# Kernel optimization log

Measured on AMD Instinct MI355X. Metric: run time of the kernel, lower is better.

## Reference

```python
import jax, jax.numpy as jnp
import numpy as np

NUM_HEADS = 8
HEAD_DIM = 64
WIN = (8, 8, 8)  # (wT, wH, wW)


def setup_inputs() -> dict:
    key = jax.random.key(0)
    k1, k2, k3 = jax.random.split(key, 3)
    B, T, H, W, C = 2, 16, 32, 32, 512
    d_inner = NUM_HEADS * HEAD_DIM  # 512
    x = jax.random.normal(k1, (B, T * H * W, C), dtype=jnp.float32)
    # torch Linear weights stored transposed as [in, out] for y = x @ w
    w_qkv = jax.random.normal(k2, (C, 3 * d_inner), dtype=jnp.float32) * (C ** -0.5)
    w_proj = jax.random.normal(k3, (d_inner, C), dtype=jnp.float32) * (d_inner ** -0.5)
    b_proj = jnp.zeros((C,), dtype=jnp.float32)
    return {"x": x, "w_qkv": w_qkv, "w_proj": w_proj, "b_proj": b_proj,
            "T": T, "H": H, "W": W}


def reference(x, w_qkv, w_proj, b_proj, T, H, W):
    B, N, C = x.shape
    wT, wH, wW = WIN
    scale = HEAD_DIM ** -0.5
    # module re-derives T if N mismatches T*H*W
    if N != T * H * W:
        T = N // (H * W)
    xv = x.reshape(B, T, H, W, C)
    pt, ph, pw = (-T) % wT, (-H) % wH, (-W) % wW
    if pt or ph or pw:
        xv = jnp.pad(xv, ((0, 0), (0, pt), (0, ph), (0, pw), (0, 0)))
    Tp, Hp, Wp = T + pt, H + ph, W + pw
    nT, nH, nW = Tp // wT, Hp // wH, Wp // wW
    L = wT * wH * wW  # tokens per window
    # window partition: [B*nT*nH*nW, L, C]
    xw = xv.reshape(B, nT, wT, nH, wH, nW, wW, C)
    xw = xw.transpose(0, 1, 3, 5, 2, 4, 6, 7).reshape(-1, L, C)
    # qkv projection (no bias)
    qkv = xw @ w_qkv  # [nw, L, 3*nh*hd]
    q, k, v = jnp.split(qkv, 3, axis=-1)

    def heads(t):
        return t.reshape(t.shape[0], L, NUM_HEADS, HEAD_DIM).transpose(0, 2, 1, 3)

    q, k, v = heads(q), heads(k), heads(v)  # [nw, h, L, d]
    attn = jax.nn.softmax(jnp.einsum('nhid,nhjd->nhij', q, k) * scale, axis=-1)
    o = jnp.einsum('nhij,nhjd->nhid', attn, v)
    o = o.transpose(0, 2, 1, 3).reshape(-1, L, NUM_HEADS * HEAD_DIM)
    o = o @ w_proj + b_proj  # output projection
    # window un-partition
    o = o.reshape(B, nT, nH, nW, wT, wH, wW, C)
    o = o.transpose(0, 1, 4, 2, 5, 3, 6, 7).reshape(B, Tp, Hp, Wp, C)
    return o[:, :T, :H, :W].reshape(B, N, C)
```

## Files before the change

### kernel.cpp

```cpp
#include <hip/hip_runtime.h>
#include <hip/hip_bf16.h>

typedef __hip_bfloat16 bf16;
typedef __attribute__((ext_vector_type(8))) short bf16x8;
typedef __attribute__((ext_vector_type(4))) float f32x4;

#define MROWS 32768
#define CDIM 512
#define SEL_STRIDE (512*512*64)

__device__ __forceinline__ int win_to_src_row(int m) {
  int win = m >> 9, l = m & 511;
  int b = win >> 5, rr = win & 31;
  int nt = rr >> 4, nh = (rr >> 2) & 3, nw = rr & 3;
  int wt = l >> 6, wh = (l >> 3) & 7, ww = l & 7;
  int tt = nt * 8 + wt, hh = nh * 8 + wh, wp = nw * 8 + ww;
  return (b << 14) + (tt << 10) + (hh << 5) + wp;
}

__device__ __forceinline__ unsigned short bf16bits(bf16 h) {
  return __builtin_bit_cast(unsigned short, h);
}

__device__ __forceinline__ int xcd_chunk(int bx, int n) {
  return (bx & 7) * (n >> 3) + (bx >> 3);
}

__global__ __launch_bounds__(256) void transpose_cvt_kernel(
    const float* __restrict__ src, bf16* __restrict__ dst, int R, int C) {
  __shared__ float tile[32][33];
  int bc = blockIdx.x * 32, br = blockIdx.y * 32;
  int tx = threadIdx.x, ty = threadIdx.y;
#pragma unroll
  for (int i = 0; i < 32; i += 8)
    tile[ty + i][tx] = src[(size_t)(br + ty + i) * C + bc + tx];
  __syncthreads();
#pragma unroll
  for (int i = 0; i < 32; i += 8)
    dst[(size_t)(bc + ty + i) * R + br + tx] = __float2bfloat16(tile[tx][ty + i]);
}

__global__ __launch_bounds__(256) void perm_x_kernel(const float* __restrict__ x,
                                                     bf16* __restrict__ xw) {
  const int total = MROWS * (CDIM / 4);
  for (int i = blockIdx.x * 256 + threadIdx.x; i < total; i += 2048 * 256) {
    int m = i >> 7, c4 = (i & 127) * 4;
    int src = win_to_src_row(m);
    float4 v = *(const float4*)(x + (size_t)src * CDIM + c4);
    ushort4 o;
    o.x = bf16bits(__float2bfloat16(v.x));
    o.y = bf16bits(__float2bfloat16(v.y));
    o.z = bf16bits(__float2bfloat16(v.z));
    o.w = bf16bits(__float2bfloat16(v.w));
    *(ushort4*)(xw + (size_t)m * CDIM + c4) = o;
  }
}

#define BM 128
#define BN 128
#define BK 64

__device__ __forceinline__ void gload16(const bf16* g, bf16* l) {
  __builtin_amdgcn_global_load_lds(
      (const __attribute__((address_space(1))) unsigned int*)g,
      (__attribute__((address_space(3))) unsigned int*)l, 16, 0, 0);
}

template <int MODE>
__global__ __launch_bounds__(256) void gemm_bt_kernel(
    const bf16* __restrict__ A, const bf16* __restrict__ Bt, int Ntiles,
    bf16* __restrict__ qkv_out, float* __restrict__ out,
    const float* __restrict__ bias) {
  __shared__ __align__(16) bf16 Asl[BM * BK];
  __shared__ __align__(16) bf16 Bsl[BN * BK];
  const int K = 512;
  int l2 = xcd_chunk(blockIdx.x, gridDim.x);
  int bn = (l2 >> 3) % Ntiles;
  int bm = (l2 & 7) + (l2 / (8 * Ntiles)) * 8;
  int t = threadIdx.x, lane = t & 63, w = t >> 6;
  int wr = w >> 1, wc = w & 1;
  int l15 = lane & 15, lh = lane >> 4;
  f32x4 acc[4][4] = {};

  for (int kt = 0; kt < K; kt += BK) {
    __syncthreads();
#pragma unroll
    for (int i = 0; i < 4; ++i) {
      int f = i * 256 + t;
      int row = f >> 3, cb = f & 7;
      gload16(A + (size_t)(bm * BM + row) * K + kt + cb * 8,
              &Asl[(i * 256 + w * 64) * 8]);
    }
#pragma unroll
    for (int i = 0; i < 4; ++i) {
      int f = i * 256 + t;
      int row = f >> 3, cb = f & 7;
      gload16(Bt + (size_t)(bn * BN + row) * K + kt + cb * 8,
              &Bsl[(i * 256 + w * 64) * 8]);
    }
    __syncthreads();
#pragma unroll
    for (int kk = 0; kk < 2; ++kk) {
      bf16x8 af[4], bfr[4];
#pragma unroll
      for (int mi = 0; mi < 4; ++mi)
        af[mi] = *(const bf16x8*)&Asl[(wr * 64 + mi * 16 + l15) * BK + kk * 32 + lh * 8];
#pragma unroll
      for (int nj = 0; nj < 4; ++nj)
        bfr[nj] = *(const bf16x8*)&Bsl[(wc * 64 + nj * 16 + l15) * BK + kk * 32 + lh * 8];
#pragma unroll
      for (int mi = 0; mi < 4; ++mi)
#pragma unroll
        for (int nj = 0; nj < 4; ++nj)
          acc[mi][nj] = __builtin_amdgcn_mfma_f32_16x16x32_bf16(
              af[mi], bfr[nj], acc[mi][nj], 0, 0, 0);
    }
  }

  if (MODE == 0) {
#pragma unroll
    for (int mi = 0; mi < 4; ++mi) {
      int row = bm * BM + wr * 64 + mi * 16 + lh * 4;
      int win = row >> 9, tok = row & 511;
#pragma unroll
      for (int nj = 0; nj < 4; ++nj) {
        int col = bn * BN + wc * 64 + nj * 16 + l15;
        int sel = col >> 9, cc = col & 511;
        int head = cc >> 6, d = cc & 63;
        if (sel == 2) {
          ushort4 pk;
          pk.x = bf16bits(__float2bfloat16(acc[mi][nj][0]));
          pk.y = bf16bits(__float2bfloat16(acc[mi][nj][1]));
          pk.z = bf16bits(__float2bfloat16(acc[mi][nj][2]));
          pk.w = bf16bits(__float2bfloat16(acc[mi][nj][3]));
          *(ushort4*)(qkv_out + 2 * (size_t)SEL_STRIDE +
                      (((size_t)(win * 8 + head)) * 64 + d) * 512 + tok) = pk;
        } else {
          size_t base = (size_t)sel * SEL_STRIDE +
                        (((size_t)(win * 8 + head)) * 512 + tok) * 64 + d;
#pragma unroll
          for (int r = 0; r < 4; ++r)
            qkv_out[base + (size_t)r * 64] = __float2bfloat16(acc[mi][nj][r]);
        }
      }
    }
  } else {
#pragma unroll
    for (int mi = 0; mi < 4; ++mi) {
      int row = bm * BM + wr * 64 + mi * 16 + lh * 4;
#pragma unroll
      for (int r = 0; r < 4; ++r) {
        int srow = win_to_src_row(row + r);
        float* op = out + (size_t)srow * CDIM;
#pragma unroll
        for (int nj = 0; nj < 4; ++nj) {
          int col = bn * BN + wc * 64 + nj * 16 + l15;
          op[col] = acc[mi][nj][r] + bias[col];
        }
      }
    }
  }
}

__global__ __launch_bounds__(256, 2) void attn_kernel(const bf16* __restrict__ qkv_ws,
                                                      bf16* __restrict__ o_ws) {
  __shared__ __align__(16) bf16 Pl[4][4][16 * 64];
  int l2 = xcd_chunk(blockIdx.x, 1024);
  int wh = l2 >> 1, qc = l2 & 1;
  int win = wh >> 3, head = wh & 7;
  int t = threadIdx.x, lane = t & 63, w = t >> 6;
  int l15 = lane & 15, lh = lane >> 4;
  const bf16* qb = qkv_ws + (size_t)wh * (512 * 64);
  const bf16* kb = qb + SEL_STRIDE;
  const bf16* vtb = qkv_ws + 2 * (size_t)SEL_STRIDE + (size_t)wh * (64 * 512);

  const float c_scale = 0.18033688011112042f;
  int q0 = qc * 256 + w * 64;
  bf16x8 qf[4][2];
#pragma unroll
  for (int qi = 0; qi < 4; ++qi)
#pragma unroll
    for (int kk = 0; kk < 2; ++kk)
      qf[qi][kk] = *(const bf16x8*)(qb + (size_t)(q0 + qi * 16 + l15) * 64 + kk * 32 + lh * 8);

  f32x4 acco[4][4] = {};
  float lsum[4][4] = {};
  for (int kt = 0; kt < 8; ++kt) {
    bf16x8 kf[4][2], vf[4][2];
#pragma unroll
    for (int kj = 0; kj < 4; ++kj) {
      int tok = kt * 64 + kj * 16 + l15;
#pragma unroll
      for (int kk = 0; kk < 2; ++kk)
        kf[kj][kk] = *(const bf16x8*)(kb + (size_t)tok * 64 + kk * 32 + lh * 8);
    }
#pragma unroll
    for (int nj = 0; nj < 4; ++nj) {
      int d = nj * 16 + l15;
#pragma unroll
      for (int kk = 0; kk < 2; ++kk)
        vf[nj][kk] = *(const bf16x8*)(vtb + (size_t)d * 512 + kt * 64 + kk * 32 + lh * 8);
    }
#pragma unroll
    for (int qi = 0; qi < 4; ++qi) {
      f32x4 s[4] = {};
#pragma unroll
      for (int kj = 0; kj < 4; ++kj)
#pragma unroll
        for (int kk = 0; kk < 2; ++kk)
          s[kj] = __builtin_amdgcn_mfma_f32_16x16x32_bf16(qf[qi][kk], kf[kj][kk], s[kj], 0, 0, 0);
#pragma unroll
      for (int kj = 0; kj < 4; ++kj)
#pragma unroll
        for (int r = 0; r < 4; ++r) {
          float p = __builtin_exp2f(s[kj][r] * c_scale);
          s[kj][r] = p;
          lsum[qi][r] += p;
        }
#pragma unroll
      for (int kj = 0; kj < 4; ++kj)
#pragma unroll
        for (int r = 0; r < 4; ++r) {
          int prow = lh * 4 + r, pcol = kj * 16 + l15;
          *(bf16*)((char*)&Pl[w][qi][0] + prow * 128 + ((pcol * 2) ^ ((prow & 7) << 4))) =
              __float2bfloat16(s[kj][r]);
        }
      bf16x8 pa[2];
#pragma unroll
      for (int kk = 0; kk < 2; ++kk)
        pa[kk] = *(const bf16x8*)((const char*)&Pl[w][qi][0] + l15 * 128 +
                                  ((kk * 64 + lh * 16) ^ ((l15 & 7) << 4)));
#pragma unroll
      for (int nj = 0; nj < 4; ++nj)
#pragma unroll
        for (int kk = 0; kk < 2; ++kk)
          acco[qi][nj] = __builtin_amdgcn_mfma_f32_16x16x32_bf16(pa[kk], vf[nj][kk],
                                                                 acco[qi][nj], 0, 0, 0);
    }
  }
#pragma unroll
  for (int qi = 0; qi < 4; ++qi) {
    float inv[4];
#pragma unroll
    for (int r = 0; r < 4; ++r) {
      float v = lsum[qi][r];
      v += __shfl_xor(v, 1);
      v += __shfl_xor(v, 2);
      v += __shfl_xor(v, 4);
      v += __shfl_xor(v, 8);
      inv[r] = __frcp_rn(v);
    }
#pragma unroll
    for (int nj = 0; nj < 4; ++nj)
#pragma unroll
      for (int r = 0; r < 4; ++r) {
        int row = q0 + qi * 16 + lh * 4 + r;
        int d = nj * 16 + l15;
        o_ws[((size_t)win * 512 + row) * 512 + head * 64 + d] =
            __float2bfloat16(acco[qi][nj][r] * inv[r]);
      }
  }
}

extern "C" void kernel_launch(void* const* d_in, const int* in_sizes, int n_in,
                              void* d_out, int out_size, void* d_ws, size_t ws_size,
                              hipStream_t stream) {
  const float* x = (const float*)d_in[0];
  const float* w_qkv = (const float*)d_in[1];
  const float* w_proj = (const float*)d_in[2];
  const float* b_proj = (const float*)d_in[3];
  float* out = (float*)d_out;

  const size_t OFF_QKV = 33554432;
  const size_t OFF_WQ = OFF_QKV + 100663296;
  const size_t OFF_WP = OFF_WQ + 1572864;
  const size_t NEED = OFF_WP + 524288;
  if (ws_size < NEED) return;

  char* ws = (char*)d_ws;
  bf16* xw = (bf16*)ws;
  bf16* qkv = (bf16*)(ws + OFF_QKV);
  bf16* wqkvT = (bf16*)(ws + OFF_WQ);
  bf16* wprojT = (bf16*)(ws + OFF_WP);
  bf16* o_ws = xw;

  transpose_cvt_kernel<<<dim3(1536 / 32, 512 / 32), dim3(32, 8), 0, stream>>>(w_qkv, wqkvT, 512, 1536);
  transpose_cvt_kernel<<<dim3(512 / 32, 512 / 32), dim3(32, 8), 0, stream>>>(w_proj, wprojT, 512, 512);
  perm_x_kernel<<<2048, 256, 0, stream>>>(x, xw);
  gemm_bt_kernel<0><<<256 * 12, 256, 0, stream>>>(xw, wqkvT, 12, qkv, nullptr, nullptr);
  attn_kernel<<<1024, 256, 0, stream>>>(qkv, o_ws);
  gemm_bt_kernel<1><<<256 * 4, 256, 0, stream>>>(o_ws, wprojT, 4, nullptr, out, b_proj);
}
```

Baseline: 233.3 us.

## Fuse QKV projection into attention kernel, keeping Q/K/V in LDS

Replaces the separate QKV GEMM plus attention kernels with one kernel per (window, head) that computes Q, K and V from the permuted input straight into shared memory, then runs the attention. This removes the round trip of a large bf16 QKV intermediate through global memory and one launch. In exchange each block re-reads the whole window's input twice, there are only 512 blocks of 512 threads using 160KB of LDS, and there is no cross-head reuse of the input tiles.

```diff
diff --git a/kernel.cpp b/kernel.cpp
--- a/kernel.cpp
+++ b/kernel.cpp
@@ -7,7 +7,6 @@
 
 #define MROWS 32768
 #define CDIM 512
-#define SEL_STRIDE (512*512*64)
 
 __device__ __forceinline__ int win_to_src_row(int m) {
   int win = m >> 9, l = m & 511;
@@ -20,6 +19,15 @@
 
 __device__ __forceinline__ unsigned short bf16bits(bf16 h) {
   return __builtin_bit_cast(unsigned short, h);
+}
+
+__device__ __forceinline__ ushort4 pack4(f32x4 a) {
+  ushort4 o;
+  o.x = bf16bits(__float2bfloat16(a[0]));
+  o.y = bf16bits(__float2bfloat16(a[1]));
+  o.z = bf16bits(__float2bfloat16(a[2]));
+  o.w = bf16bits(__float2bfloat16(a[3]));
+  return o;
 }
 
 __device__ __forceinline__ int xcd_chunk(int bx, int n) {
@@ -56,21 +64,203 @@
   }
 }
 
+__device__ __forceinline__ void gload16(const bf16* g, const bf16* l) {
+  __builtin_amdgcn_global_load_lds(
+      (const __attribute__((address_space(1))) unsigned int*)g,
+      (__attribute__((address_space(3))) unsigned int*)l, 16, 0, 0);
+}
+
+__global__ __launch_bounds__(512, 2) void fused_qkv_attn_kernel(
+    const bf16* __restrict__ xw, const bf16* __restrict__ wqkvT,
+    bf16* __restrict__ o_ws) {
+  __shared__ __align__(16) char smem[163840];
+  bf16* Xl = (bf16*)smem;
+  char* Kl = smem + 32768;
+  char* Vl = smem + 98304;
+  char* Ql = Vl;
+
+  int wh = xcd_chunk(blockIdx.x, 512);
+  int win = wh >> 3, head = wh & 7;
+  int t = threadIdx.x, lane = t & 63, w = t >> 6;
+  int l15 = lane & 15, lh = lane >> 4;
+  const bf16* xb = xw + (size_t)win * (512 * 512);
+
+  f32x4 aqk[8][4] = {};
+  for (int kt = 0; kt < 16; ++kt) {
+    bf16x8 aW[8];
+#pragma unroll
+    for (int mi = 0; mi < 8; ++mi) {
+      int wrow = (mi < 4 ? head * 64 + mi * 16 : 512 + head * 64 + (mi - 4) * 16) + l15;
+      aW[mi] = *(const bf16x8*)(wqkvT + (size_t)wrow * 512 + kt * 32 + lh * 8);
+    }
+    __syncthreads();
+#pragma unroll
+    for (int i = 0; i < 4; ++i) {
+      int f = i * 512 + t;
+      int row = f >> 2, cb = f & 3;
+      gload16(xb + (size_t)row * 512 + kt * 32 + (cb ^ (row & 3)) * 8,
+              (const bf16*)((char*)Xl + (i * 512 + w * 64) * 16));
+    }
+    __syncthreads();
+    bf16x8 bX[4];
+#pragma unroll
+    for (int ti = 0; ti < 4; ++ti) {
+      int row = w * 64 + ti * 16 + l15;
+      bX[ti] = *(const bf16x8*)((const char*)Xl + row * 64 + ((lh * 16) ^ ((row & 3) << 4)));
+    }
+#pragma unroll
+    for (int mi = 0; mi < 8; ++mi)
+#pragma unroll
+      for (int ti = 0; ti < 4; ++ti)
+        aqk[mi][ti] = __builtin_amdgcn_mfma_f32_16x16x32_bf16(aW[mi], bX[ti], aqk[mi][ti], 0, 0, 0);
+  }
+#pragma unroll
+  for (int mi = 0; mi < 8; ++mi)
+#pragma unroll
+    for (int ti = 0; ti < 4; ++ti) {
+      int tok = w * 64 + ti * 16 + l15;
+      int d0 = (mi & 3) * 16 + lh * 4;
+      char* base = (mi < 4) ? Ql : Kl;
+      *(ushort4*)(base + tok * 128 + ((d0 * 2) ^ ((tok & 7) << 4))) = pack4(aqk[mi][ti]);
+    }
+  __syncthreads();
+  bf16x8 qf[4][2];
+#pragma unroll
+  for (int qi = 0; qi < 4; ++qi) {
+    int tok = w * 64 + qi * 16 + l15;
+#pragma unroll
+    for (int kk = 0; kk < 2; ++kk)
+      qf[qi][kk] = *(const bf16x8*)(Ql + tok * 128 + ((kk * 64 + lh * 16) ^ ((tok & 7) << 4)));
+  }
+  __syncthreads();
+
+  f32x4 av[4][4] = {};
+  for (int kt = 0; kt < 16; ++kt) {
+    bf16x8 bW[4];
+#pragma unroll
+    for (int nj = 0; nj < 4; ++nj) {
+      int wrow = 1024 + head * 64 + nj * 16 + l15;
+      bW[nj] = *(const bf16x8*)(wqkvT + (size_t)wrow * 512 + kt * 32 + lh * 8);
+    }
+    __syncthreads();
+#pragma unroll
+    for (int i = 0; i < 4; ++i) {
+      int f = i * 512 + t;
+      int row = f >> 2, cb = f & 3;
+      gload16(xb + (size_t)row * 512 + kt * 32 + (cb ^ (row & 3)) * 8,
+              (const bf16*)((char*)Xl + (i * 512 + w * 64) * 16));
+    }
+    __syncthreads();
+    bf16x8 aX[4];
+#pragma unroll
+    for (int ti = 0; ti < 4; ++ti) {
+      int row = w * 64 + ti * 16 + l15;
+      aX[ti] = *(const bf16x8*)((const char*)Xl + row * 64 + ((lh * 16) ^ ((row & 3) << 4)));
+    }
+#pragma unroll
+    for (int ti = 0; ti < 4; ++ti)
+#pragma unroll
+      for (int nj = 0; nj < 4; ++nj)
+        av[ti][nj] = __builtin_amdgcn_mfma_f32_16x16x32_bf16(aX[ti], bW[nj], av[ti][nj], 0, 0, 0);
+  }
+#pragma unroll
+  for (int ti = 0; ti < 4; ++ti)
+#pragma unroll
+    for (int nj = 0; nj < 4; ++nj) {
+      int d = nj * 16 + l15;
+      int tok0 = w * 64 + ti * 16 + lh * 4;
+      *(ushort4*)(Vl + d * 1024 + ((tok0 * 2) ^ ((d & 7) << 4))) = pack4(av[ti][nj]);
+    }
+  __syncthreads();
+
+  const float c_scale = 0.18033688011112042f;
+  int q0 = w * 64;
+  f32x4 acco[4][4] = {};
+  float lsum[4][4] = {};
+  for (int kt = 0; kt < 8; ++kt) {
+    bf16x8 kf[4][2], vf[4][2];
+#pragma unroll
+    for (int kj = 0; kj < 4; ++kj) {
+      int tok = kt * 64 + kj * 16 + l15;
+#pragma unroll
+      for (int kk = 0; kk < 2; ++kk)
+        kf[kj][kk] = *(const bf16x8*)(Kl + tok * 128 + ((kk * 64 + lh * 16) ^ ((tok & 7) << 4)));
+    }
+#pragma unroll
+    for (int nj = 0; nj < 4; ++nj) {
+      int d = nj * 16 + l15;
+#pragma unroll
+      for (int kk = 0; kk < 2; ++kk)
+        vf[nj][kk] = *(const bf16x8*)(Vl + d * 1024 + ((kt * 128 + kk * 64 + lh * 16) ^ ((d & 7) << 4)));
+    }
+#pragma unroll
+    for (int qi = 0; qi < 4; ++qi) {
+      f32x4 s[4] = {};
+#pragma unroll
+      for (int kj = 0; kj < 4; ++kj)
+#pragma unroll
+        for (int kk = 0; kk < 2; ++kk)
+          s[kj] = __builtin_amdgcn_mfma_f32_16x16x32_bf16(qf[qi][kk], kf[kj][kk], s[kj], 0, 0, 0);
+#pragma unroll
+      for (int kj = 0; kj < 4; ++kj)
+#pragma unroll
+        for (int r = 0; r < 4; ++r) {
+          float p = __builtin_exp2f(s[kj][r] * c_scale);
+          s[kj][r] = p;
+          lsum[qi][r] += p;
+        }
+      char* myP = smem + w * 4096 + (qi & 1) * 2048;
+#pragma unroll
+      for (int kj = 0; kj < 4; ++kj)
+#pragma unroll
+        for (int r = 0; r < 4; ++r) {
+          int prow = lh * 4 + r, pcol = kj * 16 + l15;
+          *(bf16*)(myP + prow * 128 + ((pcol * 2) ^ ((prow & 7) << 4))) =
+              __float2bfloat16(s[kj][r]);
+        }
+      bf16x8 pa[2];
+#pragma unroll
+      for (int kk = 0; kk < 2; ++kk)
+        pa[kk] = *(const bf16x8*)(myP + l15 * 128 + ((kk * 64 + lh * 16) ^ ((l15 & 7) << 4)));
+#pragma unroll
+      for (int nj = 0; nj < 4; ++nj)
+#pragma unroll
+        for (int kk = 0; kk < 2; ++kk)
+          acco[qi][nj] = __builtin_amdgcn_mfma_f32_16x16x32_bf16(pa[kk], vf[nj][kk],
+                                                                 acco[qi][nj], 0, 0, 0);
+    }
+  }
+#pragma unroll
+  for (int qi = 0; qi < 4; ++qi) {
+    float inv[4];
+#pragma unroll
+    for (int r = 0; r < 4; ++r) {
+      float v = lsum[qi][r];
+      v += __shfl_xor(v, 1);
+      v += __shfl_xor(v, 2);
+      v += __shfl_xor(v, 4);
+      v += __shfl_xor(v, 8);
+      inv[r] = __frcp_rn(v);
+    }
+#pragma unroll
+    for (int nj = 0; nj < 4; ++nj)
+#pragma unroll
+      for (int r = 0; r < 4; ++r) {
+        int row = q0 + qi * 16 + lh * 4 + r;
+        int d = nj * 16 + l15;
+        o_ws[((size_t)win * 512 + row) * 512 + head * 64 + d] =
+            __float2bfloat16(acco[qi][nj][r] * inv[r]);
+      }
+  }
+}
+
 #define BM 128
 #define BN 128
 #define BK 64
 
-__device__ __forceinline__ void gload16(const bf16* g, bf16* l) {
-  __builtin_amdgcn_global_load_lds(
-      (const __attribute__((address_space(1))) unsigned int*)g,
-      (__attribute__((address_space(3))) unsigned int*)l, 16, 0, 0);
-}
-
-template <int MODE>
-__global__ __launch_bounds__(256) void gemm_bt_kernel(
+__global__ __launch_bounds__(256) void proj_gemm_kernel(
     const bf16* __restrict__ A, const bf16* __restrict__ Bt, int Ntiles,
-    bf16* __restrict__ qkv_out, float* __restrict__ out,
-    const float* __restrict__ bias) {
+    float* __restrict__ out, const float* __restrict__ bias) {
   __shared__ __align__(16) bf16 Asl[BM * BK];
   __shared__ __align__(16) bf16 Bsl[BN * BK];
   const int K = 512;
@@ -88,15 +278,13 @@
     for (int i = 0; i < 4; ++i) {
       int f = i * 256 + t;
       int row = f >> 3, cb = f & 7;
-      gload16(A + (size_t)(bm * BM + row) * K + kt + cb * 8,
-              &Asl[(i * 256 + w * 64) * 8]);
+      gload16(A + (size_t)(bm * BM + row) * K + kt + cb * 8, &Asl[(i * 256 + w * 64) * 8]);
     }
 #pragma unroll
     for (int i = 0; i < 4; ++i) {
       int f = i * 256 + t;
       int row = f >> 3, cb = f & 7;
-      gload16(Bt + (size_t)(bn * BN + row) * K + kt + cb * 8,
-              &Bsl[(i * 256 + w * 64) * 8]);
+      gload16(Bt + (size_t)(bn * BN + row) * K + kt + cb * 8, &Bsl[(i * 256 + w * 64) * 8]);
     }
     __syncthreads();
 #pragma unroll
@@ -112,153 +300,22 @@
       for (int mi = 0; mi < 4; ++mi)
 #pragma unroll
         for (int nj = 0; nj < 4; ++nj)
-          acc[mi][nj] = __builtin_amdgcn_mfma_f32_16x16x32_bf16(
-              af[mi], bfr[nj], acc[mi][nj], 0, 0, 0);
-    }
-  }
-
-  if (MODE == 0) {
-#pragma unroll
-    for (int mi = 0; mi < 4; ++mi) {
-      int row = bm * BM + wr * 64 + mi * 16 + lh * 4;
-      int win = row >> 9, tok = row & 511;
+          acc[mi][nj] = __builtin_amdgcn_mfma_f32_16x16x32_bf16(af[mi], bfr[nj], acc[mi][nj], 0, 0, 0);
+    }
+  }
+#pragma unroll
+  for (int mi = 0; mi < 4; ++mi) {
+    int row = bm * BM + wr * 64 + mi * 16 + lh * 4;
+#pragma unroll
+    for (int r = 0; r < 4; ++r) {
+      int srow = win_to_src_row(row + r);
+      float* op = out + (size_t)srow * CDIM;
 #pragma unroll
       for (int nj = 0; nj < 4; ++nj) {
         int col = bn * BN + wc * 64 + nj * 16 + l15;
-        int sel = col >> 9, cc = col & 511;
-        int head = cc >> 6, d = cc & 63;
-        if (sel == 2) {
-          ushort4 pk;
-          pk.x = bf16bits(__float2bfloat16(acc[mi][nj][0]));
-          pk.y = bf16bits(__float2bfloat16(acc[mi][nj][1]));
-          pk.z = bf16bits(__float2bfloat16(acc[mi][nj][2]));
-          pk.w = bf16bits(__float2bfloat16(acc[mi][nj][3]));
-          *(ushort4*)(qkv_out + 2 * (size_t)SEL_STRIDE +
-                      (((size_t)(win * 8 + head)) * 64 + d) * 512 + tok) = pk;
-        } else {
-          size_t base = (size_t)sel * SEL_STRIDE +
-                        (((size_t)(win * 8 + head)) * 512 + tok) * 64 + d;
-#pragma unroll
-          for (int r = 0; r < 4; ++r)
-            qkv_out[base + (size_t)r * 64] = __float2bfloat16(acc[mi][nj][r]);
-        }
+        op[col] = acc[mi][nj][r] + bias[col];
       }
     }
-  } else {
-#pragma unroll
-    for (int mi = 0; mi < 4; ++mi) {
-      int row = bm * BM + wr * 64 + mi * 16 + lh * 4;
-#pragma unroll
-      for (int r = 0; r < 4; ++r) {
-        int srow = win_to_src_row(row + r);
-        float* op = out + (size_t)srow * CDIM;
-#pragma unroll
-        for (int nj = 0; nj < 4; ++nj) {
-          int col = bn * BN + wc * 64 + nj * 16 + l15;
-          op[col] = acc[mi][nj][r] + bias[col];
-        }
-      }
-    }
-  }
-}
-
-__global__ __launch_bounds__(256, 2) void attn_kernel(const bf16* __restrict__ qkv_ws,
-                                                      bf16* __restrict__ o_ws) {
-  __shared__ __align__(16) bf16 Pl[4][4][16 * 64];
-  int l2 = xcd_chunk(blockIdx.x, 1024);
-  int wh = l2 >> 1, qc = l2 & 1;
-  int win = wh >> 3, head = wh & 7;
-  int t = threadIdx.x, lane = t & 63, w = t >> 6;
-  int l15 = lane & 15, lh = lane >> 4;
-  const bf16* qb = qkv_ws + (size_t)wh * (512 * 64);
-  const bf16* kb = qb + SEL_STRIDE;
-  const bf16* vtb = qkv_ws + 2 * (size_t)SEL_STRIDE + (size_t)wh * (64 * 512);
-
-  const float c_scale = 0.18033688011112042f;
-  int q0 = qc * 256 + w * 64;
-  bf16x8 qf[4][2];
-#pragma unroll
-  for (int qi = 0; qi < 4; ++qi)
-#pragma unroll
-    for (int kk = 0; kk < 2; ++kk)
-      qf[qi][kk] = *(const bf16x8*)(qb + (size_t)(q0 + qi * 16 + l15) * 64 + kk * 32 + lh * 8);
-
-  f32x4 acco[4][4] = {};
-  float lsum[4][4] = {};
-  for (int kt = 0; kt < 8; ++kt) {
-    bf16x8 kf[4][2], vf[4][2];
-#pragma unroll
-    for (int kj = 0; kj < 4; ++kj) {
-      int tok = kt * 64 + kj * 16 + l15;
-#pragma unroll
-      for (int kk = 0; kk < 2; ++kk)
-        kf[kj][kk] = *(const bf16x8*)(kb + (size_t)tok * 64 + kk * 32 + lh * 8);
-    }
-#pragma unroll
-    for (int nj = 0; nj < 4; ++nj) {
-      int d = nj * 16 + l15;
-#pragma unroll
-      for (int kk = 0; kk < 2; ++kk)
-        vf[nj][kk] = *(const bf16x8*)(vtb + (size_t)d * 512 + kt * 64 + kk * 32 + lh * 8);
-    }
-#pragma unroll
-    for (int qi = 0; qi < 4; ++qi) {
-      f32x4 s[4] = {};
-#pragma unroll
-      for (int kj = 0; kj < 4; ++kj)
-#pragma unroll
-        for (int kk = 0; kk < 2; ++kk)
-          s[kj] = __builtin_amdgcn_mfma_f32_16x16x32_bf16(qf[qi][kk], kf[kj][kk], s[kj], 0, 0, 0);
-#pragma unroll
-      for (int kj = 0; kj < 4; ++kj)
-#pragma unroll
-        for (int r = 0; r < 4; ++r) {
-          float p = __builtin_exp2f(s[kj][r] * c_scale);
-          s[kj][r] = p;
-          lsum[qi][r] += p;
-        }
-#pragma unroll
-      for (int kj = 0; kj < 4; ++kj)
-#pragma unroll
-        for (int r = 0; r < 4; ++r) {
-          int prow = lh * 4 + r, pcol = kj * 16 + l15;
-          *(bf16*)((char*)&Pl[w][qi][0] + prow * 128 + ((pcol * 2) ^ ((prow & 7) << 4))) =
-              __float2bfloat16(s[kj][r]);
-        }
-      bf16x8 pa[2];
-#pragma unroll
-      for (int kk = 0; kk < 2; ++kk)
-        pa[kk] = *(const bf16x8*)((const char*)&Pl[w][qi][0] + l15 * 128 +
-                                  ((kk * 64 + lh * 16) ^ ((l15 & 7) << 4)));
-#pragma unroll
-      for (int nj = 0; nj < 4; ++nj)
-#pragma unroll
-        for (int kk = 0; kk < 2; ++kk)
-          acco[qi][nj] = __builtin_amdgcn_mfma_f32_16x16x32_bf16(pa[kk], vf[nj][kk],
-                                                                 acco[qi][nj], 0, 0, 0);
-    }
-  }
-#pragma unroll
-  for (int qi = 0; qi < 4; ++qi) {
-    float inv[4];
-#pragma unroll
-    for (int r = 0; r < 4; ++r) {
-      float v = lsum[qi][r];
-      v += __shfl_xor(v, 1);
-      v += __shfl_xor(v, 2);
-      v += __shfl_xor(v, 4);
-      v += __shfl_xor(v, 8);
-      inv[r] = __frcp_rn(v);
-    }
-#pragma unroll
-    for (int nj = 0; nj < 4; ++nj)
-#pragma unroll
-      for (int r = 0; r < 4; ++r) {
-        int row = q0 + qi * 16 + lh * 4 + r;
-        int d = nj * 16 + l15;
-        o_ws[((size_t)win * 512 + row) * 512 + head * 64 + d] =
-            __float2bfloat16(acco[qi][nj][r] * inv[r]);
-      }
   }
 }
 
@@ -271,23 +328,21 @@
   const float* b_proj = (const float*)d_in[3];
   float* out = (float*)d_out;
 
-  const size_t OFF_QKV = 33554432;
-  const size_t OFF_WQ = OFF_QKV + 100663296;
+  const size_t OFF_O = 33554432;
+  const size_t OFF_WQ = OFF_O + 33554432;
   const size_t OFF_WP = OFF_WQ + 1572864;
   const size_t NEED = OFF_WP + 524288;
   if (ws_size < NEED) return;
 
   char* ws = (char*)d_ws;
   bf16* xw = (bf16*)ws;
-  bf16* qkv = (bf16*)(ws + OFF_QKV);
+  bf16* o_ws = (bf16*)(ws + OFF_O);
   bf16* wqkvT = (bf16*)(ws + OFF_WQ);
   bf16* wprojT = (bf16*)(ws + OFF_WP);
-  bf16* o_ws = xw;
 
   transpose_cvt_kernel<<<dim3(1536 / 32, 512 / 32), dim3(32, 8), 0, stream>>>(w_qkv, wqkvT, 512, 1536);
   transpose_cvt_kernel<<<dim3(512 / 32, 512 / 32), dim3(32, 8), 0, stream>>>(w_proj, wprojT, 512, 512);
   perm_x_kernel<<<2048, 256, 0, stream>>>(x, xw);
-  gemm_bt_kernel<0><<<256 * 12, 256, 0, stream>>>(xw, wqkvT, 12, qkv, nullptr, nullptr);
-  attn_kernel<<<1024, 256, 0, stream>>>(qkv, o_ws);
-  gemm_bt_kernel<1><<<256 * 4, 256, 0, stream>>>(o_ws, wprojT, 4, nullptr, out, b_proj);
-}
+  fused_qkv_attn_kernel<<<512, 512, 0, stream>>>(xw, wqkvT, o_ws);
+  proj_gemm_kernel<<<1024, 256, 0, stream>>>(o_ws, wprojT, 4, out, b_proj);
+}
```

Result: slower. 250.9 us (+7.5%).
